# Optimization experiments

Hardware: AMD Instinct MI355X
Metric: run time of the kernel (lower is better)

The kernel has to match this reference:

```python
import jax, jax.numpy as jnp
import numpy as np

RADIUS = 3
OUT = 16
EPS = 1e-5


def setup_inputs() -> dict:
    key = jax.random.key(0)
    ks = jax.random.split(key, 20)
    N, E, EL, IN, OUT2 = 100000, 1600000, 6400000, 16, 2 * OUT
    inp = {
        "x": jax.random.normal(ks[0], (N, IN), jnp.float32),
        "y": jax.random.normal(ks[1], (E, IN), jnp.float32),
        "deg_g": jax.random.uniform(ks[2], (N, 1), jnp.float32),
        "deg_lg": jax.random.uniform(ks[3], (E, 1), jnp.float32),
        "theta_W": jax.random.normal(ks[4], (3 + RADIUS, OUT2, IN), jnp.float32) * 0.1,
        "theta_b": jax.random.normal(ks[5], (3 + RADIUS, OUT2), jnp.float32) * 0.1,
        "gamma_W": jax.random.normal(ks[6], (3 + RADIUS, OUT2, IN), jnp.float32) * 0.1,
        "gamma_b": jax.random.normal(ks[7], (3 + RADIUS, OUT2), jnp.float32) * 0.1,
        "bn_x_w": jnp.ones((OUT,), jnp.float32),
        "bn_x_b": jnp.zeros((OUT,), jnp.float32),
        "bn_y_w": jnp.ones((OUT,), jnp.float32),
        "bn_y_b": jnp.zeros((OUT,), jnp.float32),
        "src_g": jax.random.randint(ks[8], (E,), 0, N, jnp.int32),
        "dst_g": jax.random.randint(ks[9], (E,), 0, N, jnp.int32),
        "src_lg": jax.random.randint(ks[10], (EL,), 0, E, jnp.int32),
        "dst_lg": jax.random.randint(ks[11], (EL,), 0, E, jnp.int32),
        "eid2nid": jax.random.randint(ks[12], (E,), 0, N, jnp.int32),
    }
    return inp


def _spmm(z, src, dst, n):
    # copy_src + sum: out[v] = sum_{(u,v) in edges} z[u]
    return jax.ops.segment_sum(z[src], dst, num_segments=n)


def _aggregate(z, src, dst, n, radius):
    zl = []
    z = _spmm(z, src, dst, n)
    zl.append(z)
    for i in range(radius - 1):
        for _ in range(2 ** i):
            z = _spmm(z, src, dst, n)
        zl.append(z)
    return zl


def _lin(z, W, b):
    return z @ W.T + b


def _bn(h, w, b):
    m = h.mean(axis=0)
    v = h.var(axis=0)  # biased, as torch BN training normalization
    return (h - m) * jax.lax.rsqrt(v + EPS) * w + b


def reference(x, y, deg_g, deg_lg, theta_W, theta_b, gamma_W, gamma_b,
              bn_x_w, bn_x_b, bn_y_w, bn_y_b,
              src_g, dst_g, src_lg, dst_lg, eid2nid):
    N, E = x.shape[0], y.shape[0]
    # edge -> source-node feature gather (F.embedding)
    xy = x[eid2nid]
    # node branch
    x_list = [_lin(z, theta_W[3 + i], theta_b[3 + i])
              for i, z in enumerate(_aggregate(x, src_g, dst_g, N, RADIUS))]
    yx = jax.ops.segment_sum(y, dst_g, num_segments=N)  # copy_edge + sum
    xn = (_lin(x, theta_W[0], theta_b[0])
          + _lin(deg_g * x, theta_W[1], theta_b[1])
          + sum(x_list)
          + _lin(yx, theta_W[2], theta_b[2]))
    x_out = _bn(xn[:, :OUT] + jax.nn.relu(xn[:, OUT:]), bn_x_w, bn_x_b)
    # line-graph (edge) branch
    y_list = [_lin(z, gamma_W[3 + i], gamma_b[3 + i])
              for i, z in enumerate(_aggregate(y, src_lg, dst_lg, E, RADIUS))]
    xy_agg = _spmm(xy, src_lg, dst_lg, E)
    yn = (_lin(y, gamma_W[0], gamma_b[0])
          + _lin(deg_lg * y, gamma_W[1], gamma_b[1])
          + sum(y_list)
          + _lin(xy_agg, gamma_W[2], gamma_b[2]))
    y_out = _bn(yn[:, :OUT] + jax.nn.relu(yn[:, OUT:]), bn_y_w, bn_y_b)
    return (x_out, y_out)
```

## Files before the change

### kernel.cpp

```cpp
#include <hip/hip_runtime.h>
#include <stdint.h>

typedef __attribute__((ext_vector_type(8))) short bfx8;
typedef __attribute__((ext_vector_type(4))) float f32x4;

__device__ __forceinline__ float bf2f(unsigned short u){
  union { unsigned int i; float f; } x; x.i = ((unsigned int)u) << 16; return x.f;
}
__device__ __forceinline__ unsigned short f2bf(float f){
  union { float f; unsigned int i; } x; x.f = f;
  unsigned int r = x.i + 0x7fff + ((x.i >> 16) & 1);
  return (unsigned short)(r >> 16);
}
__device__ __forceinline__ void unpack8(uint4 v, float* o){
  o[0]=bf2f((unsigned short)(v.x)); o[1]=bf2f((unsigned short)(v.x>>16));
  o[2]=bf2f((unsigned short)(v.y)); o[3]=bf2f((unsigned short)(v.y>>16));
  o[4]=bf2f((unsigned short)(v.z)); o[5]=bf2f((unsigned short)(v.z>>16));
  o[6]=bf2f((unsigned short)(v.w)); o[7]=bf2f((unsigned short)(v.w>>16));
}
__device__ __forceinline__ uint4 pack8(const float* f){
  uint4 v;
  v.x = (unsigned)f2bf(f[0]) | ((unsigned)f2bf(f[1])<<16);
  v.y = (unsigned)f2bf(f[2]) | ((unsigned)f2bf(f[3])<<16);
  v.z = (unsigned)f2bf(f[4]) | ((unsigned)f2bf(f[5])<<16);
  v.w = (unsigned)f2bf(f[6]) | ((unsigned)f2bf(f[7])<<16);
  return v;
}
__device__ __forceinline__ void loadrow16_f32(const float* p, float* in){
  float4 a = *(const float4*)p;      float4 b = *(const float4*)(p+4);
  float4 c = *(const float4*)(p+8);  float4 d = *(const float4*)(p+12);
  in[0]=a.x; in[1]=a.y; in[2]=a.z; in[3]=a.w;
  in[4]=b.x; in[5]=b.y; in[6]=b.z; in[7]=b.w;
  in[8]=c.x; in[9]=c.y; in[10]=c.z; in[11]=c.w;
  in[12]=d.x; in[13]=d.y; in[14]=d.z; in[15]=d.w;
}
__device__ __forceinline__ bfx8 f32x8_to_bf(const float* p, float m){
  float4 a = *(const float4*)p; float4 b = *(const float4*)(p+4);
  bfx8 r;
  r[0]=(short)f2bf(a.x*m); r[1]=(short)f2bf(a.y*m); r[2]=(short)f2bf(a.z*m); r[3]=(short)f2bf(a.w*m);
  r[4]=(short)f2bf(b.x*m); r[5]=(short)f2bf(b.y*m); r[6]=(short)f2bf(b.z*m); r[7]=(short)f2bf(b.w*m);
  return r;
}

__global__ void k_f2b(const float* __restrict__ src, unsigned short* __restrict__ dst, long n8){
  long t = (long)blockIdx.x*blockDim.x + threadIdx.x;
  if (t >= n8) return;
  const float* p = src + t*8;
  float4 a = *(const float4*)p; float4 b = *(const float4*)(p+4);
  float f[8] = {a.x,a.y,a.z,a.w,b.x,b.y,b.z,b.w};
  *(uint4*)(dst + t*8) = pack8(f);
}

__global__ void __launch_bounds__(256) k_bcount(
    const int* __restrict__ dst, int n, int chunk, int shift, int nb,
    int* __restrict__ bkt_cnt){
  extern __shared__ int hist[];
  for (int b = threadIdx.x; b < nb; b += 256) hist[b] = 0;
  __syncthreads();
  int i0 = blockIdx.x * chunk;
  int iend = min(i0 + chunk, n);
  for (int i = i0 + threadIdx.x; i < iend; i += 256)
    atomicAdd(&hist[dst[i] >> shift], 1);
  __syncthreads();
  for (int b = threadIdx.x; b < nb; b += 256){
    int h = hist[b];
    if (h) atomicAdd(&bkt_cnt[b], h);
  }
}

__global__ void k_bscan(const int* __restrict__ bkt_cnt, int* __restrict__ bkt_base,
                        int* __restrict__ bcur, int nb){
  __shared__ int s[256];
  __shared__ int carry;
  if (threadIdx.x==0) carry = 0;
  __syncthreads();
  for (int base=0; base<nb; base+=256){
    int i = base + threadIdx.x;
    int v = (i<nb) ? bkt_cnt[i] : 0;
    s[threadIdx.x] = v; __syncthreads();
    for (int off=1; off<256; off<<=1){
      int t = (threadIdx.x>=off) ? s[threadIdx.x-off] : 0;
      __syncthreads();
      s[threadIdx.x] += t;
      __syncthreads();
    }
    int excl = s[threadIdx.x] - v + carry;
    if (i<nb){ bkt_base[i] = excl; bcur[i*16] = excl; }
    int tot = s[255];
    __syncthreads();
    if (threadIdx.x==0) carry += tot;
    __syncthreads();
  }
  if (threadIdx.x==0) bkt_base[nb] = carry;
}

template<int PAY, int CHUNK, int NBMAX>
__global__ void __launch_bounds__(256) k_scatter2(
    const int* __restrict__ src, const int* __restrict__ dst, int n,
    int shift, int nb, int* __restrict__ bcur, int* __restrict__ out){
  __shared__ int hist[NBMAX];
  __shared__ int delta[NBMAX];
  __shared__ int s[256];
  __shared__ int slot[CHUNK];
  __shared__ int carry;
  for (int b = threadIdx.x; b < nb; b += 256) hist[b] = 0;
  if (threadIdx.x==0) carry = 0;
  __syncthreads();
  int i0 = blockIdx.x * CHUNK;
  int iend = min(i0 + CHUNK, n);
  for (int i = i0 + threadIdx.x; i < iend; i += 256)
    atomicAdd(&hist[dst[i] >> shift], 1);
  __syncthreads();
  for (int base = 0; base < nb; base += 256){
    int b = base + threadIdx.x;
    int v = (b < nb) ? hist[b] : 0;
    s[threadIdx.x] = v; __syncthreads();
    for (int off=1; off<256; off<<=1){
      int t = (threadIdx.x>=off) ? s[threadIdx.x-off] : 0;
      __syncthreads();
      s[threadIdx.x] += t;
      __syncthreads();
    }
    int excl = s[threadIdx.x] - v + carry;
    int tot = s[255];
    if (b < nb){
      int g = v ? atomicAdd(&bcur[b*16], v) : 0;
      delta[b] = g - excl;
      hist[b] = excl;
    }
    __syncthreads();
    if (threadIdx.x==0) carry += tot;
    __syncthreads();
  }
  for (int i = i0 + threadIdx.x; i < iend; i += 256){
    int b = dst[i] >> shift;
    int p = atomicAdd(&hist[b], 1);
    slot[p] = i;
  }
  __syncthreads();
  int cnt = iend - i0;
  for (int j = threadIdx.x; j < cnt; j += 256){
    int i = slot[j];
    int d = dst[i];
    int b = d >> shift;
    int a = j + delta[b];
    if (PAY == 2) *(int2*)(out + (size_t)a*2) = make_int2(d, src[i]);
    else          *(int4*)(out + (size_t)a*4) = make_int4(d, src[i], i, 0);
  }
}

template<bool EID, int RLOG>
__global__ void __launch_bounds__(256) k_place2(
    const int* __restrict__ bkt_base, const int* __restrict__ binned,
    int nrows, int* __restrict__ rowptr,
    int* __restrict__ colA, int* __restrict__ colB){
  constexpr int R = 1 << RLOG;
  constexpr int K = R / 256;
  __shared__ int cnt[R];
  __shared__ int s[256];
  int rowBase = blockIdx.x << RLOG;
  int nr = min(R, nrows - rowBase);
  int beg = bkt_base[blockIdx.x], end = bkt_base[blockIdx.x+1];
  #pragma unroll
  for (int k=0;k<K;k++) cnt[threadIdx.x + k*256] = 0;
  __syncthreads();
  for (int i = beg + threadIdx.x; i < end; i += 256){
    int d = EID ? ((const int4*)binned)[i].x : ((const int2*)binned)[i].x;
    atomicAdd(&cnt[d & (R-1)], 1);
  }
  __syncthreads();
  int myBase = threadIdx.x * K;
  int part = 0;
  #pragma unroll
  for (int k=0;k<K;k++) part += cnt[myBase+k];
  s[threadIdx.x] = part; __syncthreads();
  for (int off=1; off<256; off<<=1){
    int t = (threadIdx.x>=off) ? s[threadIdx.x-off] : 0;
    __syncthreads();
    s[threadIdx.x] += t;
    __syncthreads();
  }
  int run = s[threadIdx.x] - part + beg;
  #pragma unroll
  for (int k=0;k<K;k++){
    int idx = myBase + k;
    int c = cnt[idx];
    cnt[idx] = run;
    if (idx < nr) rowptr[rowBase + idx] = run;
    run += c;
  }
  if (blockIdx.x == gridDim.x-1 && threadIdx.x == 255) rowptr[nrows] = end;
  __syncthreads();
  for (int i = beg + threadIdx.x; i < end; i += 256){
    if (EID){
      int4 v = ((const int4*)binned)[i];
      int p = atomicAdd(&cnt[v.x & (R-1)], 1);
      colA[p] = v.y; colB[p] = v.z;
    } else {
      int2 v = ((const int2*)binned)[i];
      int p = atomicAdd(&cnt[v.x & (R-1)], 1);
      colA[p] = v.y;
    }
  }
}

template<bool REMAP>
__global__ void __launch_bounds__(256) k_spmm(
    const int* __restrict__ rowptr, const int* __restrict__ col,
    const int* __restrict__ remap,
    const unsigned short* __restrict__ src, unsigned short* __restrict__ out, int nrows){
  int t = blockIdx.x*256 + threadIdx.x;
  int row = t >> 1, half = t & 1;
  if (row >= nrows) return;
  int beg = rowptr[row], end = rowptr[row+1];
  float acc[8] = {0,0,0,0,0,0,0,0};
  float acc2[8] = {0,0,0,0,0,0,0,0};
  const unsigned short* sp = src + (half<<3);
  int i = beg;
  for (; i+2 <= end; i += 2){
    int c0 = col[i], c1 = col[i+1];
    if (REMAP){ c0 = remap[c0]; c1 = remap[c1]; }
    uint4 v0 = *(const uint4*)(sp + ((size_t)c0<<4));
    uint4 v1 = *(const uint4*)(sp + ((size_t)c1<<4));
    float f0[8], f1[8]; unpack8(v0, f0); unpack8(v1, f1);
    #pragma unroll
    for (int j=0;j<8;j++){ acc[j] += f0[j]; acc2[j] += f1[j]; }
  }
  if (i < end){
    int c = col[i];
    if (REMAP) c = remap[c];
    uint4 v = *(const uint4*)(sp + ((size_t)c<<4));
    float f[8]; unpack8(v, f);
    #pragma unroll
    for (int j=0;j<8;j++) acc[j] += f[j];
  }
  #pragma unroll
  for (int j=0;j<8;j++) acc[j] += acc2[j];
  *(uint4*)(out + ((size_t)row<<4) + (half<<3)) = pack8(acc);
}

__global__ void __launch_bounds__(256) k_final_mfma(
    const float* __restrict__ base, const float* __restrict__ deg,
    const unsigned short* __restrict__ s2, const unsigned short* __restrict__ s3,
    const unsigned short* __restrict__ s4, const unsigned short* __restrict__ s5,
    const float* __restrict__ W, const float* __restrict__ Bb,
    float* __restrict__ hout, int nrows){
  int lane = threadIdx.x & 63;
  int l15 = lane & 15;
  int quad = lane >> 4;
  int kbase = quad * 8;
  int slocal = kbase >> 4;
  int k0 = kbase & 15;

  bfx8 bh[3][2], bl[3][2];
  #pragma unroll
  for (int kb=0; kb<3; ++kb){
    int s = kb*2 + slocal;
    #pragma unroll
    for (int t=0;t<2;++t){
      int o = t*16 + l15;
      const float* wp = W + s*512 + o*16 + k0;
      bfx8 hi, lo;
      #pragma unroll
      for (int j=0;j<8;j++){
        float w0 = wp[j];
        unsigned short h = f2bf(w0);
        unsigned short l2 = f2bf(w0 - bf2f(h));
        hi[j] = (short)h; lo[j] = (short)l2;
      }
      bh[kb][t] = hi; bl[kb][t] = lo;
    }
  }
  float bias0 = 0.f, bias1 = 0.f;
  #pragma unroll
  for (int s=0;s<6;s++){ bias0 += Bb[s*32 + l15]; bias1 += Bb[s*32 + 16 + l15]; }

  int ntiles = (nrows + 15) >> 4;
  int wstart = (blockIdx.x<<2) + (threadIdx.x>>6);
  int wstep  = gridDim.x<<2;
  for (int tile = wstart; tile < ntiles; tile += wstep){
    int R0 = tile << 4;
    int row = R0 + l15;
    int rowc = min(row, nrows-1);
    size_t ro = (size_t)rowc*16 + k0;
    float m = slocal ? deg[rowc] : 1.f;
    bfx8 a0 = f32x8_to_bf(base + ro, m);
    bfx8 a1 = *(const bfx8*)((slocal ? s3 : s2) + ro);
    bfx8 a2 = *(const bfx8*)((slocal ? s5 : s4) + ro);
    f32x4 c0 = {bias0,bias0,bias0,bias0};
    f32x4 c1 = {bias1,bias1,bias1,bias1};
    c0 = __builtin_amdgcn_mfma_f32_16x16x32_bf16(a0, bh[0][0], c0, 0,0,0);
    c1 = __builtin_amdgcn_mfma_f32_16x16x32_bf16(a0, bh[0][1], c1, 0,0,0);
    c0 = __builtin_amdgcn_mfma_f32_16x16x32_bf16(a1, bh[1][0], c0, 0,0,0);
    c1 = __builtin_amdgcn_mfma_f32_16x16x32_bf16(a1, bh[1][1], c1, 0,0,0);
    c0 = __builtin_amdgcn_mfma_f32_16x16x32_bf16(a2, bh[2][0], c0, 0,0,0);
    c1 = __builtin_amdgcn_mfma_f32_16x16x32_bf16(a2, bh[2][1], c1, 0,0,0);
    c0 = __builtin_amdgcn_mfma_f32_16x16x32_bf16(a0, bl[0][0], c0, 0,0,0);
    c1 = __builtin_amdgcn_mfma_f32_16x16x32_bf16(a0, bl[0][1], c1, 0,0,0);
    c0 = __builtin_amdgcn_mfma_f32_16x16x32_bf16(a1, bl[1][0], c0, 0,0,0);
    c1 = __builtin_amdgcn_mfma_f32_16x16x32_bf16(a1, bl[1][1], c1, 0,0,0);
    c0 = __builtin_amdgcn_mfma_f32_16x16x32_bf16(a2, bl[2][0], c0, 0,0,0);
    c1 = __builtin_amdgcn_mfma_f32_16x16x32_bf16(a2, bl[2][1], c1, 0,0,0);
    #pragma unroll
    for (int j=0;j<4;j++){
      int r = R0 + quad*4 + j;
      if (r < nrows) hout[(size_t)r*16 + l15] = c0[j] + fmaxf(c1[j], 0.f);
    }
  }
}

__global__ void __launch_bounds__(256) k_red(
    const float* __restrict__ h, int nrows, float* __restrict__ stats){
  __shared__ float redS[4][16];
  __shared__ float redQ[4][16];
  float ssum[16], ssq[16];
  #pragma unroll
  for (int c=0;c<16;c++){ ssum[c]=0.f; ssq[c]=0.f; }
  for (long r = (long)blockIdx.x*256 + threadIdx.x; r < nrows; r += (long)gridDim.x*256){
    float in[16];
    loadrow16_f32(h + r*16, in);
    #pragma unroll
    for (int c=0;c<16;c++){ ssum[c] += in[c]; ssq[c] += in[c]*in[c]; }
  }
  int lane = threadIdx.x & 63, wid = threadIdx.x >> 6;
  #pragma unroll
  for (int c=0;c<16;c++){
    float s = ssum[c], q = ssq[c];
    for (int off=32; off; off>>=1){ s += __shfl_xor(s, off, 64); q += __shfl_xor(q, off, 64); }
    if (lane==0){ redS[wid][c] = s; redQ[wid][c] = q; }
  }
  __syncthreads();
  if (threadIdx.x < 16){
    float s=0.f, q=0.f;
    #pragma unroll
    for (int w4=0; w4<4; w4++){ s += redS[w4][threadIdx.x]; q += redQ[w4][threadIdx.x]; }
    atomicAdd(&stats[threadIdx.x], s);
    atomicAdd(&stats[16 + threadIdx.x], q);
  }
}

__global__ void k_stats(const float* __restrict__ st,
                        const float* __restrict__ wx, const float* __restrict__ bx,
                        const float* __restrict__ wy, const float* __restrict__ by,
                        float* __restrict__ prm, int nx, int ny){
  int c = threadIdx.x;
  if (c < 16){
    float m  = st[c]/(float)nx;
    float v  = st[16+c]/(float)nx - m*m;
    float sc = wx[c] * rsqrtf(v + 1e-5f);
    prm[c] = sc; prm[16+c] = bx[c] - m*sc;
    float m2  = st[32+c]/(float)ny;
    float v2  = st[48+c]/(float)ny - m2*m2;
    float sc2 = wy[c] * rsqrtf(v2 + 1e-5f);
    prm[32+c] = sc2; prm[48+c] = by[c] - m2*sc2;
  }
}

__global__ void k_norm(float* __restrict__ out, const float* __restrict__ prm,
                       long nx, long ntot){
  long g = ((long)blockIdx.x*256 + threadIdx.x) * 8;
  if (g >= ntot) return;
  const float* p = (g < nx) ? prm : prm + 32;
  int cbase = (int)(g & 15);
  float4 a = *(float4*)(out + g);
  float4 b = *(float4*)(out + g + 4);
  float f[8] = {a.x,a.y,a.z,a.w,b.x,b.y,b.z,b.w};
  #pragma unroll
  for (int j=0;j<8;j++){ int c = cbase + j; f[j] = f[j]*p[c] + p[16+c]; }
  *(float4*)(out + g)     = make_float4(f[0],f[1],f[2],f[3]);
  *(float4*)(out + g + 4) = make_float4(f[4],f[5],f[6],f[7]);
}

extern "C" void kernel_launch(void* const* d_in, const int* in_sizes, int n_in,
                              void* d_out, int out_size, void* d_ws, size_t ws_size,
                              hipStream_t stream){
  const float* x      = (const float*)d_in[0];
  const float* y      = (const float*)d_in[1];
  const float* deg_g  = (const float*)d_in[2];
  const float* deg_lg = (const float*)d_in[3];
  const float* thW    = (const float*)d_in[4];
  const float* thB    = (const float*)d_in[5];
  const float* gaW    = (const float*)d_in[6];
  const float* gaB    = (const float*)d_in[7];
  const float* bnxw   = (const float*)d_in[8];
  const float* bnxb   = (const float*)d_in[9];
  const float* bnyw   = (const float*)d_in[10];
  const float* bnyb   = (const float*)d_in[11];
  const int* src_g   = (const int*)d_in[12];
  const int* dst_g   = (const int*)d_in[13];
  const int* src_lg  = (const int*)d_in[14];
  const int* dst_lg  = (const int*)d_in[15];
  const int* eid2nid = (const int*)d_in[16];

  const int N  = in_sizes[2];
  const int E  = in_sizes[3];
  const int EL = in_sizes[14];

  char* w = (char*)d_ws;
  auto alloc = [&](size_t bytes)->void*{
    void* p = (void*)w; w += (bytes + 255) & ~(size_t)255; return p;
  };
  int* g_rowptr   = (int*)alloc((size_t)(N+1)*4);
  int* g_col_src  = (int*)alloc((size_t)E*4);
  int* g_col_eid  = (int*)alloc((size_t)E*4);
  int* lg_rowptr  = (int*)alloc((size_t)(E+1)*4);
  int* lg_col     = (int*)alloc((size_t)EL*4);
  int* bcur       = (int*)alloc((size_t)1024*16*4);
  int* bkt_cnt_g  = (int*)alloc(1024*4);
  int* bkt_base_g = (int*)alloc(1025*4);
  int* bkt_cnt_l  = (int*)alloc(1024*4);
  int* bkt_base_l = (int*)alloc(1025*4);
  float* stats    = (float*)alloc(64*4);
  float* prm      = (float*)alloc(64*4);
  unsigned short* xb  = (unsigned short*)alloc((size_t)N*16*2);
  unsigned short* nz1 = (unsigned short*)alloc((size_t)N*16*2);
  unsigned short* nz2 = (unsigned short*)alloc((size_t)N*16*2);
  unsigned short* nz3 = (unsigned short*)alloc((size_t)N*16*2);
  unsigned short* nz4 = (unsigned short*)alloc((size_t)N*16*2);
  unsigned short* nyx = (unsigned short*)alloc((size_t)N*16*2);
  unsigned short* eb1 = (unsigned short*)alloc((size_t)E*16*2);
  unsigned short* eb2 = (unsigned short*)alloc((size_t)E*16*2);
  unsigned short* eb3 = (unsigned short*)alloc((size_t)E*16*2);
  unsigned short* yb  = (unsigned short*)alloc((size_t)E*16*2);
  unsigned short* eb4 = yb;
  int* binned_g = (int*)eb1;
  int* binned_l = (int*)eb2;

  hipMemsetAsync(bkt_cnt_g, 0, 1024*4, stream);
  hipMemsetAsync(bkt_cnt_l, 0, 1024*4, stream);
  hipMemsetAsync(stats, 0, 64*4, stream);

  long nx8 = (long)N*16/8, ny8 = (long)E*16/8;
  k_f2b<<<(int)((nx8+255)/256), 256, 0, stream>>>(x, xb, nx8);
  k_f2b<<<(int)((ny8+255)/256), 256, 0, stream>>>(y, yb, ny8);

  const int RLOG_G = 8;
  int nb_g = (N + (1<<RLOG_G) - 1) >> RLOG_G;
  k_bcount<<<(E+8191)/8192, 256, (size_t)nb_g*4, stream>>>(
      dst_g, E, 8192, RLOG_G, nb_g, bkt_cnt_g);
  k_bscan<<<1, 256, 0, stream>>>(bkt_cnt_g, bkt_base_g, bcur, nb_g);
  k_scatter2<4, 4096, 512><<<(E+4095)/4096, 256, 0, stream>>>(
      src_g, dst_g, E, RLOG_G, nb_g, bcur, binned_g);
  k_place2<true, RLOG_G><<<nb_g, 256, 0, stream>>>(
      bkt_base_g, binned_g, N, g_rowptr, g_col_src, g_col_eid);

  const int RLOG_L = 11;
  int nb_l = (E + (1<<RLOG_L) - 1) >> RLOG_L;
  k_bcount<<<(EL+16383)/16384, 256, (size_t)nb_l*4, stream>>>(
      dst_lg, EL, 16384, RLOG_L, nb_l, bkt_cnt_l);
  k_bscan<<<1, 256, 0, stream>>>(bkt_cnt_l, bkt_base_l, bcur, nb_l);
  k_scatter2<2, 16384, 1024><<<(EL+16383)/16384, 256, 0, stream>>>(
      src_lg, dst_lg, EL, RLOG_L, nb_l, bcur, binned_l);
  k_place2<false, RLOG_L><<<nb_l, 256, 0, stream>>>(
      bkt_base_l, binned_l, E, lg_rowptr, lg_col, (int*)nullptr);

  int gs = (2*N+255)/256;
  int es = (2*E+255)/256;
  k_spmm<false><<<es, 256, 0, stream>>>(lg_rowptr, lg_col, nullptr, yb,  eb1, E);
  k_spmm<false><<<gs, 256, 0, stream>>>(g_rowptr, g_col_eid, nullptr, yb, nyx, N);
  k_spmm<false><<<gs, 256, 0, stream>>>(g_rowptr, g_col_src, nullptr, xb,  nz1, N);
  k_spmm<false><<<gs, 256, 0, stream>>>(g_rowptr, g_col_src, nullptr, nz1, nz2, N);
  k_spmm<false><<<gs, 256, 0, stream>>>(g_rowptr, g_col_src, nullptr, nz2, nz3, N);
  k_spmm<false><<<gs, 256, 0, stream>>>(g_rowptr, g_col_src, nullptr, nz3, nz4, N);
  k_spmm<false><<<es, 256, 0, stream>>>(lg_rowptr, lg_col, nullptr, eb1, eb2, E);
  k_spmm<false><<<es, 256, 0, stream>>>(lg_rowptr, lg_col, nullptr, eb2, eb3, E);
  k_spmm<false><<<es, 256, 0, stream>>>(lg_rowptr, lg_col, nullptr, eb3, eb4, E);
  k_spmm<true><<<es, 256, 0, stream>>>(lg_rowptr, lg_col, eid2nid, xb,  eb3, E);

  float* outp = (float*)d_out;
  int tg = (N + 15) >> 4;  int bg2 = (tg + 3) / 4;  if (bg2 > 2048) bg2 = 2048;
  int te = (E + 15) >> 4;  int be2 = (te + 3) / 4;  if (be2 > 2048) be2 = 2048;
  k_final_mfma<<<bg2, 256, 0, stream>>>(x, deg_g, nyx, nz1, nz2, nz4,
                                        thW, thB, outp, N);
  k_final_mfma<<<be2, 256, 0, stream>>>(y, deg_lg, eb3, eb1, eb2, eb4,
                                        gaW, gaB, outp + (size_t)N*16, E);

  k_red<<<512, 256, 0, stream>>>(outp, N, stats);
  k_red<<<512, 256, 0, stream>>>(outp + (size_t)N*16, E, stats + 32);
  k_stats<<<1, 64, 0, stream>>>(stats, bnxw, bnxb, bnyw, bnyb, prm, N, E);
  long ntot = (long)(N + E) * 16;
  k_norm<<<(int)((ntot/8 + 255)/256), 256, 0, stream>>>(outp, prm, (long)N*16, ntot);
}
```

Before: 1.571 ms.

## Pack binned CSR payloads into fewer words and write buckets contiguously

The bucket-scatter step now packs the local row offset into the high bits of the source index. The line graph therefore uses one 32-bit word per edge instead of two, and the node graph uses two words instead of four, which cuts binned-buffer traffic in both scatter and place. The scatter stage stores packed payloads in shared memory and writes each bucket as a contiguous run using 16-lane groups, replacing the earlier per-element indirection. The line-graph chunk size is halved to fit shared memory. Packing relies on source indices fitting in 21 or 24 bits, which holds for E=1.6M and N=100k.

```diff
diff --git a/kernel.cpp b/kernel.cpp
--- a/kernel.cpp
+++ b/kernel.cpp
@@ -94,15 +94,15 @@
   if (threadIdx.x==0) bkt_base[nb] = carry;
 }
 
-template<int PAY, int CHUNK, int NBMAX>
-__global__ void __launch_bounds__(256) k_scatter2(
+template<int CHUNK, int NBMAX, bool PACK1, int LBITS>
+__global__ void __launch_bounds__(256) k_scatter3(
     const int* __restrict__ src, const int* __restrict__ dst, int n,
     int shift, int nb, int* __restrict__ bcur, int* __restrict__ out){
   __shared__ int hist[NBMAX];
   __shared__ int delta[NBMAX];
   __shared__ int s[256];
-  __shared__ int slot[CHUNK];
   __shared__ int carry;
+  __shared__ int slotP[PACK1 ? CHUNK : 2*CHUNK];
   for (int b = threadIdx.x; b < nb; b += 256) hist[b] = 0;
   if (threadIdx.x==0) carry = 0;
   __syncthreads();
@@ -133,24 +133,28 @@
     __syncthreads();
   }
   for (int i = i0 + threadIdx.x; i < iend; i += 256){
-    int b = dst[i] >> shift;
-    int p = atomicAdd(&hist[b], 1);
-    slot[p] = i;
-  }
-  __syncthreads();
-  int cnt = iend - i0;
-  for (int j = threadIdx.x; j < cnt; j += 256){
-    int i = slot[j];
     int d = dst[i];
     int b = d >> shift;
-    int a = j + delta[b];
-    if (PAY == 2) *(int2*)(out + (size_t)a*2) = make_int2(d, src[i]);
-    else          *(int4*)(out + (size_t)a*4) = make_int4(d, src[i], i, 0);
-  }
-}
-
-template<bool EID, int RLOG>
-__global__ void __launch_bounds__(256) k_place2(
+    int p = atomicAdd(&hist[b], 1);
+    int w0 = ((d & ((1<<shift)-1)) << LBITS) | src[i];
+    if (PACK1) slotP[p] = w0;
+    else { slotP[2*p] = w0; slotP[2*p+1] = i; }
+  }
+  __syncthreads();
+  int grp = threadIdx.x >> 4, lane16 = threadIdx.x & 15;
+  for (int b = grp; b < nb; b += 16){
+    int lbeg = b ? hist[b-1] : 0;
+    int lend = hist[b];
+    int dlt  = delta[b];
+    for (int k = lbeg + lane16; k < lend; k += 16){
+      if (PACK1) out[(size_t)(k + dlt)] = slotP[k];
+      else *(int2*)(out + (size_t)(k + dlt)*2) = make_int2(slotP[2*k], slotP[2*k+1]);
+    }
+  }
+}
+
+template<int MODE, int RLOG>
+__global__ void __launch_bounds__(256) k_place3(
     const int* __restrict__ bkt_base, const int* __restrict__ binned,
     int nrows, int* __restrict__ rowptr,
     int* __restrict__ colA, int* __restrict__ colB){
@@ -165,8 +169,9 @@
   for (int k=0;k<K;k++) cnt[threadIdx.x + k*256] = 0;
   __syncthreads();
   for (int i = beg + threadIdx.x; i < end; i += 256){
-    int d = EID ? ((const int4*)binned)[i].x : ((const int2*)binned)[i].x;
-    atomicAdd(&cnt[d & (R-1)], 1);
+    int r = (MODE==0) ? (int)(((unsigned)binned[i]) >> 21)
+                      : (int)(((unsigned)((const int2*)binned)[i].x) >> 24);
+    atomicAdd(&cnt[r], 1);
   }
   __syncthreads();
   int myBase = threadIdx.x * K;
@@ -192,14 +197,15 @@
   if (blockIdx.x == gridDim.x-1 && threadIdx.x == 255) rowptr[nrows] = end;
   __syncthreads();
   for (int i = beg + threadIdx.x; i < end; i += 256){
-    if (EID){
-      int4 v = ((const int4*)binned)[i];
-      int p = atomicAdd(&cnt[v.x & (R-1)], 1);
-      colA[p] = v.y; colB[p] = v.z;
+    if (MODE==0){
+      unsigned v = (unsigned)binned[i];
+      int p = atomicAdd(&cnt[v >> 21], 1);
+      colA[p] = (int)(v & 0x1FFFFFu);
     } else {
       int2 v = ((const int2*)binned)[i];
-      int p = atomicAdd(&cnt[v.x & (R-1)], 1);
-      colA[p] = v.y;
+      unsigned w0 = (unsigned)v.x;
+      int p = atomicAdd(&cnt[w0 >> 24], 1);
+      colA[p] = (int)(w0 & 0xFFFFFFu); colB[p] = v.y;
     }
   }
 }
@@ -439,9 +445,9 @@
   k_bcount<<<(E+8191)/8192, 256, (size_t)nb_g*4, stream>>>(
       dst_g, E, 8192, RLOG_G, nb_g, bkt_cnt_g);
   k_bscan<<<1, 256, 0, stream>>>(bkt_cnt_g, bkt_base_g, bcur, nb_g);
-  k_scatter2<4, 4096, 512><<<(E+4095)/4096, 256, 0, stream>>>(
+  k_scatter3<4096, 512, false, 24><<<(E+4095)/4096, 256, 0, stream>>>(
       src_g, dst_g, E, RLOG_G, nb_g, bcur, binned_g);
-  k_place2<true, RLOG_G><<<nb_g, 256, 0, stream>>>(
+  k_place3<1, RLOG_G><<<nb_g, 256, 0, stream>>>(
       bkt_base_g, binned_g, N, g_rowptr, g_col_src, g_col_eid);
 
   const int RLOG_L = 11;
@@ -449,9 +455,9 @@
   k_bcount<<<(EL+16383)/16384, 256, (size_t)nb_l*4, stream>>>(
       dst_lg, EL, 16384, RLOG_L, nb_l, bkt_cnt_l);
   k_bscan<<<1, 256, 0, stream>>>(bkt_cnt_l, bkt_base_l, bcur, nb_l);
-  k_scatter2<2, 16384, 1024><<<(EL+16383)/16384, 256, 0, stream>>>(
+  k_scatter3<8192, 1024, true, 21><<<(EL+8191)/8192, 256, 0, stream>>>(
       src_lg, dst_lg, EL, RLOG_L, nb_l, bcur, binned_l);
-  k_place2<false, RLOG_L><<<nb_l, 256, 0, stream>>>(
+  k_place3<0, RLOG_L><<<nb_l, 256, 0, stream>>>(
       bkt_base_l, binned_l, E, lg_rowptr, lg_col, (int*)nullptr);
 
   int gs = (2*N+255)/256;
```

New measurement: 1.507 ms. 4.1% less time.
